# Kernel tuning notes

Hardware: AMD Instinct MI355X
Metric: run time of the kernel (lower is better)

The kernel has to match this reference:

```python
import jax, jax.numpy as jnp
import numpy as np

B, S, D, DEPTH = 2, 2048, 1024, 4
NUM_LEAVES = 2 ** DEPTH          # 16
NUM_DEC = NUM_LEAVES - 1         # 15


def setup_inputs() -> dict:
    key = jax.random.key(0)
    k1, k2, k3, k4, k5 = jax.random.split(key, 5)
    scale = 1.0 / np.sqrt(D)
    return {
        "x": jax.random.normal(k1, (B, S, D), dtype=jnp.float32),
        "dec_w": jax.random.normal(k2, (NUM_DEC, D), dtype=jnp.float32) * scale,
        "dec_b": jax.random.normal(k3, (NUM_DEC,), dtype=jnp.float32) * scale,
        "leaf_w": jax.random.normal(k4, (NUM_LEAVES, D, D), dtype=jnp.float32) * scale,  # [leaf, out, in] (torch Linear layout)
        "leaf_b": jax.random.normal(k5, (NUM_LEAVES, D), dtype=jnp.float32) * scale,
    }


def reference(x, dec_w, dec_b, leaf_w, leaf_b):
    num_leaves = leaf_w.shape[0]
    num_dec = num_leaves - 1
    # All decision-node sigmoids in one batched GEMM: [B,S,num_dec]
    dec = jax.nn.sigmoid(jnp.einsum("bsd,nd->bsn", x, dec_w) + dec_b)
    # Faithful to the original: each tree slot is multiplied exactly once by its
    # direct parent's decision (left child: p, right child: 1-p).
    leaf_idx = np.arange(num_dec, 2 * num_leaves - 1)      # slots holding leaf probs
    parent = (leaf_idx - 1) // 2                           # [num_leaves]
    is_left = (leaf_idx % 2 == 1)                          # [num_leaves]
    dec_p = dec[..., parent]                               # [B,S,num_leaves]
    leaf_probs = jnp.where(jnp.asarray(is_left), dec_p, 1.0 - dec_p)
    # All leaf MLPs as one batched GEMM: [B,S,L,D]
    leaf_out = jnp.einsum("bsd,lod->bslo", x, leaf_w) + leaf_b
    # Probability-weighted sum over leaves -> [B,S,D]
    return jnp.einsum("bslo,bsl->bso", leaf_out, leaf_probs)
```

## Files before the change

### kernel.cpp

```cpp
#include <hip/hip_runtime.h>
#include <stdint.h>


#define M_TOK 4096
#define DDIM  1024
#define KFLAT 9216

typedef __bf16 bf16x8 __attribute__((ext_vector_type(8)));
typedef float  f32x4  __attribute__((ext_vector_type(4)));
typedef unsigned short u16x4 __attribute__((ext_vector_type(4)));
typedef unsigned short u16x8 __attribute__((ext_vector_type(8)));

#define GLB(p) ((const __attribute__((address_space(1))) void*)(p))
#define LDS(p) ((__attribute__((address_space(3))) void*)(p))

__device__ __forceinline__ unsigned short f2bf(float f) {
    union { float f; uint32_t u; } v; v.f = f;
    uint32_t u = v.u;
    return (unsigned short)((u + 0x7fffu + ((u >> 16) & 1u)) >> 16);
}

__device__ __forceinline__ bf16x8 asbf(f32x4 v) {
    bf16x8 r; __builtin_memcpy(&r, &v, 16); return r;
}

template<int OFF>
__device__ __forceinline__ f32x4 dsr(uint32_t a) {
    f32x4 r;
    asm volatile("ds_read_b128 %0, %1 offset:%c2" : "=v"(r) : "v"(a), "i"(OFF));
    return r;
}

__global__ __launch_bounds__(256) void prep_dec_kernel(
    const float* __restrict__ x, const float* __restrict__ dec_w,
    const float* __restrict__ dec_b, const float* __restrict__ lw,
    const float* __restrict__ lb, unsigned short* __restrict__ wp,
    float* __restrict__ bw, unsigned short* __restrict__ xs,
    float* __restrict__ pmat, int newlay)
{
    if (blockIdx.x < 1024) {
        int idx = blockIdx.x * 256 + threadIdx.x;
        int o  = idx >> 8;
        int k4 = (idx & 255) << 2;
        size_t src = (size_t)o * DDIM + k4;
        const int nt = o >> 8, wn = (o >> 6) & 3, jj = (o >> 4) & 3, ra = o & 15;
        auto store4 = [&](int l, u16x4 d) {
            if (newlay) {
                int K    = l * DDIM + k4;
                int kt   = K >> 6;
                int half = (K >> 5) & 1;
                int g16  = (K >> 3) & 3;
                int e0   = K & 7;
                size_t a = ((size_t)(nt * 144 + kt) * 4 + wn) * 4096
                         + (jj * 2 + half) * 512 + (g16 * 16 + ra) * 8 + e0;
                *(u16x4*)(wp + a) = d;
            } else {
                *(u16x4*)(wp + (size_t)o * KFLAT + l * DDIM + k4) = d;
            }
        };
        float4 acc = make_float4(0.f, 0.f, 0.f, 0.f);
#pragma unroll
        for (int j = 0; j < 8; ++j) {
            const float4 a = *(const float4*)(lw + (size_t)(2*j)   * DDIM*DDIM + src);
            const float4 b = *(const float4*)(lw + (size_t)(2*j+1) * DDIM*DDIM + src);
            u16x4 d;
            d[0] = f2bf(a.x - b.x); d[1] = f2bf(a.y - b.y);
            d[2] = f2bf(a.z - b.z); d[3] = f2bf(a.w - b.w);
            store4(j, d);
            acc.x += b.x; acc.y += b.y; acc.z += b.z; acc.w += b.w;
        }
        u16x4 s;
        s[0] = f2bf(acc.x); s[1] = f2bf(acc.y); s[2] = f2bf(acc.z); s[3] = f2bf(acc.w);
        store4(8, s);
        if ((idx & 255) == 0) {
            float sb = 0.f;
#pragma unroll
            for (int j = 0; j < 8; ++j) {
                float ba = lb[(2*j) * DDIM + o];
                float bb = lb[(2*j+1) * DDIM + o];
                bw[j * DDIM + o] = ba - bb;
                sb += bb;
            }
            bw[8 * DDIM + o] = sb;
        }
    } else {
        int m    = (blockIdx.x - 1024) * 4 + (threadIdx.x >> 6);
        int lane = threadIdx.x & 63;
        const float* xr = x + (size_t)m * DDIM + lane * 16;
        float xv[16];
        *(float4*)&xv[0]  = *(const float4*)(xr + 0);
        *(float4*)&xv[4]  = *(const float4*)(xr + 4);
        *(float4*)&xv[8]  = *(const float4*)(xr + 8);
        *(float4*)&xv[12] = *(const float4*)(xr + 12);
        float s[8];
#pragma unroll
        for (int j = 0; j < 8; ++j) {
            const float* wr = dec_w + (size_t)(7 + j) * DDIM + lane * 16;
            float a = 0.f;
#pragma unroll
            for (int i = 0; i < 16; i += 4) {
                float4 wv = *(const float4*)(wr + i);
                a = fmaf(xv[i], wv.x, fmaf(xv[i+1], wv.y, fmaf(xv[i+2], wv.z, fmaf(xv[i+3], wv.w, a))));
            }
            s[j] = a;
        }
#pragma unroll
        for (int j = 0; j < 8; ++j)
#pragma unroll
            for (int off = 32; off > 0; off >>= 1)
                s[j] += __shfl_xor(s[j], off);
        float p[8];
#pragma unroll
        for (int j = 0; j < 8; ++j)
            p[j] = 1.0f / (1.0f + expf(-(s[j] + dec_b[7 + j])));
        if (lane == 0) {
#pragma unroll
            for (int j = 0; j < 8; ++j)
                pmat[(size_t)m * 8 + j] = p[j];
        }
#pragma unroll
        for (int j = 0; j < 9; ++j) {
            float pj = (j < 8) ? p[j] : 1.0f;
            unsigned short* dst = xs + (size_t)m * KFLAT + j * DDIM + lane * 16;
#pragma unroll
            for (int c = 0; c < 2; ++c) {
                u16x8 o;
#pragma unroll
                for (int e = 0; e < 8; ++e) o[e] = f2bf(pj * xv[c * 8 + e]);
                *(u16x8*)(dst + c * 8) = o;
            }
        }
    }
}

#define WAITV0 asm volatile("s_waitcnt vmcnt(0)" ::: "memory")
#define WAITV4 asm volatile("s_waitcnt vmcnt(4)" ::: "memory")
#define WAITV8 asm volatile("s_waitcnt vmcnt(8)" ::: "memory")
#define BARR   __builtin_amdgcn_s_barrier()
#define SBAR   __builtin_amdgcn_sched_barrier(0)
#define LGKM0  do { asm volatile("s_waitcnt lgkmcnt(0)" ::: "memory"); SBAR; } while(0)
#define LGKM4  do { asm volatile("s_waitcnt lgkmcnt(4)" ::: "memory"); SBAR; } while(0)

#define MFMA_Q(q, ASET, BSET) do { \
    __builtin_amdgcn_s_setprio(1); \
    _Pragma("unroll") \
    for (int mfl = 0; mfl < 2; ++mfl) { \
        _Pragma("unroll") \
        for (int j = 0; j < 4; ++j) { \
            acc[2*(q)+mfl][j] = __builtin_amdgcn_mfma_f32_16x16x32_bf16(asbf(ASET[mfl][0]), asbf(BSET[j][0]), acc[2*(q)+mfl][j], 0, 0, 0); \
            acc[2*(q)+mfl][j] = __builtin_amdgcn_mfma_f32_16x16x32_bf16(asbf(ASET[mfl][1]), asbf(BSET[j][1]), acc[2*(q)+mfl][j], 0, 0, 0); \
        } \
    } \
    __builtin_amdgcn_s_setprio(0); \
} while(0)

#define READ_A(SET, q, a0, a1) do { \
    SET[0][0] = dsr<(2*(q)+0)*2048>(a0); \
    SET[0][1] = dsr<(2*(q)+0)*2048>(a1); \
    SET[1][0] = dsr<(2*(q)+1)*2048>(a0); \
    SET[1][1] = dsr<(2*(q)+1)*2048>(a1); \
} while(0)

#define READ_B(SET, b0, b1) do { \
    SET[0][0] = dsr<0*2048>(b0); SET[0][1] = dsr<0*2048>(b1); \
    SET[1][0] = dsr<1*2048>(b0); SET[1][1] = dsr<1*2048>(b1); \
    SET[2][0] = dsr<2*2048>(b0); SET[2][1] = dsr<2*2048>(b1); \
    SET[3][0] = dsr<3*2048>(b0); SET[3][1] = dsr<3*2048>(b1); \
} while(0)

__global__ __launch_bounds__(512, 2) void tree_gemm9(
    const unsigned short* __restrict__ xs,
    const unsigned short* __restrict__ wpf,
    float* __restrict__ out, float* __restrict__ parts)
{
    extern __shared__ char smem[];
    const int tid  = threadIdx.x;
    const int lane = tid & 63;
    const int w    = tid >> 6;
    const int wm   = w >> 2, wn = w & 3;
    const int ra   = lane & 15;
    const int g16  = lane >> 4;

    const int flat = blockIdx.x;
    const int xcd  = flat & 7;
    const int idx  = flat >> 3;
    const int cc   = idx >> 4;
    const int mt   = idx & 15;
    const int code = xcd * 2 + cc;
    const int nt   = code >> 2;
    const int g    = code & 3;
    const int m0   = mt * 256, n0 = nt * 256;
    const int k0   = g * 2304;
    const int NT   = 36;

    uint32_t sbase = (uint32_t)(uintptr_t)(__attribute__((address_space(3))) char*)smem;
    const uint32_t colb0 = (uint32_t)((g16 ^ (ra & 7)) << 4);
    const uint32_t colb1 = colb0 ^ 64;
    const uint32_t baseA0s = sbase + wm * 16384 + ra * 128 + colb0;
    const uint32_t baseA1s = sbase + wm * 16384 + ra * 128 + colb1;

    const int kel = (((lane & 7) ^ (lane >> 3)) & 7) * 8;
    const int rA  = w * 8 + (lane >> 3);

    auto stageA = [&](int buf, int tt, int hh) {
        const unsigned short* s0 = xs + (size_t)(m0 + hh * 128 + rA) * KFLAT + (k0 + tt * 64 + kel);
        char* d0 = smem + buf * 32768 + hh * 16384 + w * 1024;
        __builtin_amdgcn_global_load_lds(GLB(s0), LDS(d0), 16, 0, 0);
        __builtin_amdgcn_global_load_lds(GLB(s0 + (size_t)64 * KFLAT), LDS(d0 + 8192), 16, 0, 0);
    };

    const unsigned short* bsrc = wpf
        + ((size_t)(nt * 144 + g * 36) * 4 + wn) * 4096 + lane * 8;

    f32x4 acc[8][4] = {};
    f32x4 avA[2][2], avB[2][2], bvX[4][2], bvY[4][2];

    auto loadB = [&](f32x4 (&SET)[4][2], const unsigned short* bp) {
#pragma unroll
        for (int j = 0; j < 4; ++j) {
            SET[j][0] = *(const f32x4*)(bp + (j * 2 + 0) * 512);
            SET[j][1] = *(const f32x4*)(bp + (j * 2 + 1) * 512);
        }
    };

    stageA(0, 0, 0); stageA(0, 0, 1);
    loadB(bvX, bsrc);
    WAITV0;
    BARR;
    READ_A(avA, 0, baseA0s, baseA1s);

#define TILE_BODY(T, CUR, NXT) do { \
    const int t_ = (T); \
    const bool s1 = (t_ + 1 < NT); \
    if (s1) { \
        stageA((t_ + 1) & 1, t_ + 1, 0); stageA((t_ + 1) & 1, t_ + 1, 1); \
        loadB(NXT, bsrc + 16384); \
    } \
    const uint32_t a0_ = baseA0s + ((uint32_t)(t_ & 1) << 15); \
    const uint32_t a1_ = baseA1s + ((uint32_t)(t_ & 1) << 15); \
    READ_A(avB, 1, a0_, a1_); \
    LGKM4;  MFMA_Q(0, avA, CUR); \
    READ_A(avA, 2, a0_, a1_); \
    LGKM4;  MFMA_Q(1, avB, CUR); \
    READ_A(avB, 3, a0_, a1_); \
    LGKM4;  MFMA_Q(2, avA, CUR); \
    LGKM0; \
    if (s1) { \
        WAITV0; \
        BARR; \
        const uint32_t na0_ = baseA0s + ((uint32_t)((t_ + 1) & 1) << 15); \
        const uint32_t na1_ = baseA1s + ((uint32_t)((t_ + 1) & 1) << 15); \
        READ_A(avA, 0, na0_, na1_); \
    } \
    MFMA_Q(3, avB, CUR); \
    SBAR; \
    bsrc += 16384; \
} while(0)

    for (int tp = 0; tp < NT; tp += 2) {
        TILE_BODY(tp,     bvX, bvY);
        TILE_BODY(tp + 1, bvY, bvX);
    }
#undef TILE_BODY

    float* dst = (g == 0) ? out : parts + (size_t)(g - 1) * M_TOK * DDIM;
#pragma unroll
    for (int mf = 0; mf < 8; ++mf)
#pragma unroll
        for (int e = 0; e < 4; ++e) {
            int row = m0 + wm * 128 + mf * 16 + g16 * 4 + e;
#pragma unroll
            for (int j = 0; j < 4; ++j)
                dst[(size_t)row * DDIM + n0 + wn * 64 + j * 16 + ra] = acc[mf][j][e];
        }
}

__global__ __launch_bounds__(256) void reduce2_kernel(
    float* __restrict__ out, const float* __restrict__ parts,
    const float* __restrict__ pmat, const float* __restrict__ bw, int np)
{
    size_t i = (size_t)blockIdx.x * 256 + threadIdx.x;
    int m   = (int)(i >> 8);
    int col = (int)(i & 255) * 4;
    float4 a = ((const float4*)out)[i];
    for (int p = 0; p < np; ++p) {
        float4 b = ((const float4*)(parts + (size_t)p * M_TOK * DDIM))[i];
        a.x += b.x; a.y += b.y; a.z += b.z; a.w += b.w;
    }
    float4 pa = *(const float4*)(pmat + (size_t)m * 8);
    float4 pb = *(const float4*)(pmat + (size_t)m * 8 + 4);
    float4 bias = *(const float4*)(bw + 8 * DDIM + col);
#pragma unroll
    for (int l = 0; l < 8; ++l) {
        float pl = (l < 4) ? ((const float*)&pa)[l] : ((const float*)&pb)[l - 4];
        float4 bl = *(const float4*)(bw + l * DDIM + col);
        bias.x = fmaf(pl, bl.x, bias.x); bias.y = fmaf(pl, bl.y, bias.y);
        bias.z = fmaf(pl, bl.z, bias.z); bias.w = fmaf(pl, bl.w, bias.w);
    }
    a.x += bias.x; a.y += bias.y; a.z += bias.z; a.w += bias.w;
    ((float4*)out)[i] = a;
}

__global__ __launch_bounds__(512, 2) void tree_gemm8(
    const unsigned short* __restrict__ xs, const unsigned short* __restrict__ wp,
    float* __restrict__ out, float* __restrict__ parts, int KG)
{
    extern __shared__ char smem[];
    const int tid  = threadIdx.x;
    const int lane = tid & 63;
    const int w    = tid >> 6;
    const int wm   = w >> 2, wn = w & 3;
    const int ra   = lane & 15;
    const int g16  = lane >> 4;

    const int bx  = blockIdx.x;
    const int xcd = bx & 7, ii = bx >> 3;
    const int nt  = xcd >> 1;
    const int mt  = (xcd & 1) * 8 + ii;
    const int m0  = mt * 256, n0 = nt * 256;
    const int g   = blockIdx.y;
    const int k0  = g * KG;
    const int NT  = KG >> 6;

    uint32_t sbase = (uint32_t)(uintptr_t)(__attribute__((address_space(3))) char*)smem;
    const uint32_t colb0 = (uint32_t)((g16 ^ (ra & 7)) << 4);
    const uint32_t colb1 = colb0 ^ 64;
    const uint32_t baseA0s = sbase + wm * 16384 + ra * 128 + colb0;
    const uint32_t baseA1s = sbase + wm * 16384 + ra * 128 + colb1;
    const uint32_t baseB0s = sbase + 65536 + wn * 8192 + ra * 128 + colb0;
    const uint32_t baseB1s = sbase + 65536 + wn * 8192 + ra * 128 + colb1;

    const int kel = (((lane & 7) ^ (lane >> 3)) & 7) * 8;
    const int rA  = w * 8 + (lane >> 3);

    auto stageA = [&](int buf, int tt, int hh) {
        const unsigned short* s0 = xs + (size_t)(m0 + hh * 128 + rA) * KFLAT + (k0 + tt * 64 + kel);
        char* d0 = smem + buf * 32768 + hh * 16384 + w * 1024;
        __builtin_amdgcn_global_load_lds(GLB(s0), LDS(d0), 16, 0, 0);
        __builtin_amdgcn_global_load_lds(GLB(s0 + (size_t)64 * KFLAT), LDS(d0 + 8192), 16, 0, 0);
    };
    auto stageB = [&](int buf, int tt, int hh) {
        const unsigned short* s0 = wp + (size_t)(n0 + hh * 128 + rA) * KFLAT + (k0 + tt * 64 + kel);
        char* d0 = smem + 65536 + buf * 32768 + hh * 16384 + w * 1024;
        __builtin_amdgcn_global_load_lds(GLB(s0), LDS(d0), 16, 0, 0);
        __builtin_amdgcn_global_load_lds(GLB(s0 + (size_t)64 * KFLAT), LDS(d0 + 8192), 16, 0, 0);
    };

    f32x4 acc[8][4] = {};
    f32x4 avA[2][2], avB[2][2], bvX[4][2], bvY[4][2];

    stageA(0, 0, 0); stageA(0, 0, 1);
    stageB(0, 0, 0); stageB(0, 0, 1);
    stageB(1, 1, 0); stageB(1, 1, 1);
    WAITV4;
    BARR;
    READ_B(bvX, baseB0s, baseB1s);
    READ_A(avA, 0, baseA0s, baseA1s);

    int bt1 = 1, bt2 = 2;

#define TILE_BODY8(T, CUR, NXT) do { \
    const int t_ = (T); \
    const bool s1 = (t_ + 1 < NT), s2 = (t_ + 2 < NT); \
    if (s1) { stageA((t_ + 1) & 1, t_ + 1, 0); stageA((t_ + 1) & 1, t_ + 1, 1); } \
    if (s2) { stageB(bt2, t_ + 2, 0); stageB(bt2, t_ + 2, 1); } \
    const uint32_t a0_ = baseA0s + ((uint32_t)(t_ & 1) << 15); \
    const uint32_t a1_ = baseA1s + ((uint32_t)(t_ & 1) << 15); \
    READ_A(avB, 1, a0_, a1_); \
    LGKM4;  MFMA_Q(0, avA, CUR); \
    READ_A(avA, 2, a0_, a1_); \
    LGKM4;  MFMA_Q(1, avB, CUR); \
    READ_A(avB, 3, a0_, a1_); \
    LGKM4;  MFMA_Q(2, avA, CUR); \
    LGKM0; \
    if (s1) { \
        if (s2) { WAITV4; } else { WAITV0; } \
        BARR; \
        const uint32_t nb0_ = baseB0s + (uint32_t)bt1 * 32768u; \
        const uint32_t nb1_ = baseB1s + (uint32_t)bt1 * 32768u; \
        const uint32_t na0_ = baseA0s + ((uint32_t)((t_ + 1) & 1) << 15); \
        const uint32_t na1_ = baseA1s + ((uint32_t)((t_ + 1) & 1) << 15); \
        READ_B(NXT, nb0_, nb1_); \
        READ_A(avA, 0, na0_, na1_); \
    } \
    MFMA_Q(3, avB, CUR); \
    SBAR; \
    bt1 = (bt1 == 2) ? 0 : bt1 + 1; \
    bt2 = (bt2 == 2) ? 0 : bt2 + 1; \
} while(0)

    for (int tp = 0; tp < NT; tp += 2) {
        TILE_BODY8(tp,     bvX, bvY);
        TILE_BODY8(tp + 1, bvY, bvX);
    }
#undef TILE_BODY8

    float* dst = (g == 0) ? out : parts + (size_t)(g - 1) * M_TOK * DDIM;
#pragma unroll
    for (int mf = 0; mf < 8; ++mf)
#pragma unroll
        for (int e = 0; e < 4; ++e) {
            int row = m0 + wm * 128 + mf * 16 + g16 * 4 + e;
#pragma unroll
            for (int j = 0; j < 4; ++j)
                dst[(size_t)row * DDIM + n0 + wn * 64 + j * 16 + ra] = acc[mf][j][e];
        }
}

__global__ __launch_bounds__(256, 4) void tree_gemm3(
    const unsigned short* __restrict__ xs, const unsigned short* __restrict__ wp,
    const float* __restrict__ bw, const float* __restrict__ pmat,
    float* __restrict__ out, float* __restrict__ parts, int KG)
{
    __shared__ __align__(16) unsigned short Asm[2][128 * 32];
    __shared__ __align__(16) unsigned short Bsm[2][128 * 32];
    const int tid  = threadIdx.x;
    const int lane = tid & 63;
    const int w    = tid >> 6;
    const int wm   = w >> 1, wn = w & 1;
    const int bx   = blockIdx.x;
    const int xcd  = bx & 7;
    const int ii   = bx >> 3;
    const int mt   = xcd * 4 + (ii >> 3);
    const int nt   = ii & 7;
    const int m0   = mt * 128, n0 = nt * 128;
    const int g    = blockIdx.y;
    const int k0   = g * KG;
    const int ra   = lane & 15;
    const int kb   = (lane >> 4) * 8;
    f32x4 acc[4][4] = {};
    auto stage = [&](int buf, int t) {
#pragma unroll
        for (int c = 0; c < 2; ++c) {
            int row = w * 32 + c * 16 + (lane >> 2);
            int ke  = k0 + t * 32 + (lane & 3) * 8;
            const unsigned short* ga = xs + (size_t)(m0 + row) * KFLAT + ke;
            __builtin_amdgcn_global_load_lds(GLB(ga), LDS(&Asm[buf][w * 1024 + c * 512]), 16, 0, 0);
            const unsigned short* gb = wp + (size_t)(n0 + row) * KFLAT + ke;
            __builtin_amdgcn_global_load_lds(GLB(gb), LDS(&Bsm[buf][w * 1024 + c * 512]), 16, 0, 0);
        }
    };
    const int TOT = KG >> 5;
    stage(0, 0);
    __syncthreads();
    int cur = 0;
    for (int t = 0; t < TOT; ++t) {
        if (t + 1 < TOT) stage(cur ^ 1, t + 1);
        bf16x8 av2[4], bv2[4];
#pragma unroll
        for (int i2 = 0; i2 < 4; ++i2)
            av2[i2] = *(const bf16x8*)&Asm[cur][(wm * 64 + i2 * 16 + ra) * 32 + kb];
#pragma unroll
        for (int j = 0; j < 4; ++j)
            bv2[j] = *(const bf16x8*)&Bsm[cur][(wn * 64 + j * 16 + ra) * 32 + kb];
#pragma unroll
        for (int i2 = 0; i2 < 4; ++i2)
#pragma unroll
            for (int j = 0; j < 4; ++j)
                acc[i2][j] = __builtin_amdgcn_mfma_f32_16x16x32_bf16(av2[i2], bv2[j], acc[i2][j], 0, 0, 0);
        __syncthreads();
        cur ^= 1;
    }
    float* bsm = (float*)&Asm[0][0];
    if (g == 0) {
        for (int idx = tid; idx < 9 * 128; idx += 256)
            bsm[idx] = bw[(idx >> 7) * DDIM + n0 + (idx & 127)];
    }
    __syncthreads();
    float* dst = (g == 0) ? out : parts + (size_t)(g - 1) * M_TOK * DDIM;
#pragma unroll
    for (int i2 = 0; i2 < 4; ++i2)
#pragma unroll
        for (int r = 0; r < 4; ++r) {
            int row = m0 + wm * 64 + i2 * 16 + (lane >> 4) * 4 + r;
            float4 pa, pb;
            if (g == 0) {
                pa = *(const float4*)(pmat + (size_t)row * 8);
                pb = *(const float4*)(pmat + (size_t)row * 8 + 4);
            }
#pragma unroll
            for (int j = 0; j < 4; ++j) {
                int cl = wn * 64 + j * 16 + ra;
                float v = acc[i2][j][r];
                if (g == 0) {
                    v += pa.x * bsm[0 * 128 + cl] + pa.y * bsm[1 * 128 + cl]
                       + pa.z * bsm[2 * 128 + cl] + pa.w * bsm[3 * 128 + cl]
                       + pb.x * bsm[4 * 128 + cl] + pb.y * bsm[5 * 128 + cl]
                       + pb.z * bsm[6 * 128 + cl] + pb.w * bsm[7 * 128 + cl]
                       + bsm[8 * 128 + cl];
                }
                dst[(size_t)row * DDIM + n0 + cl] = v;
            }
        }
}

__global__ __launch_bounds__(256) void reduce_kernel(
    float* __restrict__ out, const float* __restrict__ parts, int np)
{
    size_t i = (size_t)blockIdx.x * 256 + threadIdx.x;
    float4 a = ((const float4*)out)[i];
    for (int p = 0; p < np; ++p) {
        float4 b = ((const float4*)(parts + (size_t)p * M_TOK * DDIM))[i];
        a.x += b.x; a.y += b.y; a.z += b.z; a.w += b.w;
    }
    ((float4*)out)[i] = a;
}

extern "C" void kernel_launch(void* const* d_in, const int* in_sizes, int n_in,
                              void* d_out, int out_size, void* d_ws, size_t ws_size,
                              hipStream_t stream) {
    (void)in_sizes; (void)n_in; (void)out_size;
    const float* x     = (const float*)d_in[0];
    const float* dec_w = (const float*)d_in[1];
    const float* dec_b = (const float*)d_in[2];
    const float* lw    = (const float*)d_in[3];
    const float* lb    = (const float*)d_in[4];
    float* out = (float*)d_out;
    uint8_t* w8 = (uint8_t*)d_ws;

    unsigned short* xs   = (unsigned short*)(w8);
    unsigned short* wp   = (unsigned short*)(w8 + 75497472);
    float*          bw   = (float*)(w8 + 94371840);
    float*          pmat = (float*)(w8 + 94408704);
    float*          parts= (float*)(w8 + 94539776);
    const size_t NEED3 = 94539776 + 2ull * 16777216;
    const size_t NEED4 = 94539776 + 3ull * 16777216;

    int ks = (ws_size >= NEED4) ? 4 : (ws_size >= NEED3) ? 3 : 0;
    if (!ks) return;

    bool use9 = false;
    if (ks == 4) {
        hipError_t e9 = hipFuncSetAttribute(
            reinterpret_cast<const void*>(tree_gemm9),
            hipFuncAttributeMaxDynamicSharedMemorySize, 65536);
        use9 = (e9 == hipSuccess);
    }

    prep_dec_kernel<<<2048, 256, 0, stream>>>(x, dec_w, dec_b, lw, lb, wp, bw, xs, pmat,
                                              use9 ? 1 : 0);

    if (use9) {
        tree_gemm9<<<256, 512, 65536, stream>>>(xs, wp, out, parts);
        reduce2_kernel<<<4096, 256, 0, stream>>>(out, parts, pmat, bw, 3);
        return;
    }

    hipError_t e8 = hipFuncSetAttribute(
        reinterpret_cast<const void*>(tree_gemm8),
        hipFuncAttributeMaxDynamicSharedMemorySize, 163840);
    if (e8 == hipSuccess) {
        tree_gemm8<<<dim3(64, ks), 512, 163840, stream>>>(xs, wp, out, parts, KFLAT / ks);
        reduce2_kernel<<<4096, 256, 0, stream>>>(out, parts, pmat, bw, ks - 1);
    } else {
        tree_gemm3<<<dim3(256, ks), 256, 0, stream>>>(xs, wp, bw, pmat, out, parts, KFLAT / ks);
        reduce_kernel<<<4096, 256, 0, stream>>>(out, parts, ks - 1);
    }
}
```

Before: 137.2 us.

## Switch main GEMM to 32x32x16 MFMA with matching B layout and relaxed waits

Replaces the 16x16x32 MFMA GEMM kernel with a 32x32x16 variant. The prep kernel writes the packed weight layout to match the new fragment shape, and the LDS A-read swizzle is reorganized into four k-slices. The vmcnt waits are relaxed (vmcnt(12)/vmcnt(8) instead of vmcnt(0)) so global prefetch overlaps more with compute. The goal is fewer LDS reads per FLOP and higher MFMA throughput, at the cost of larger accumulator register pressure and a scattered epilogue store pattern.

```diff
diff --git a/kernel.cpp b/kernel.cpp
--- a/kernel.cpp
+++ b/kernel.cpp
@@ -8,6 +8,7 @@
 
 typedef __bf16 bf16x8 __attribute__((ext_vector_type(8)));
 typedef float  f32x4  __attribute__((ext_vector_type(4)));
+typedef float  f32x16 __attribute__((ext_vector_type(16)));
 typedef unsigned short u16x4 __attribute__((ext_vector_type(4)));
 typedef unsigned short u16x8 __attribute__((ext_vector_type(8)));
 
@@ -43,16 +44,16 @@
         int o  = idx >> 8;
         int k4 = (idx & 255) << 2;
         size_t src = (size_t)o * DDIM + k4;
-        const int nt = o >> 8, wn = (o >> 6) & 3, jj = (o >> 4) & 3, ra = o & 15;
+        const int nt = o >> 8, wn = (o >> 6) & 3, nf = (o >> 5) & 1, c31 = o & 31;
         auto store4 = [&](int l, u16x4 d) {
             if (newlay) {
-                int K    = l * DDIM + k4;
-                int kt   = K >> 6;
-                int half = (K >> 5) & 1;
-                int g16  = (K >> 3) & 3;
-                int e0   = K & 7;
+                int K  = l * DDIM + k4;
+                int kt = K >> 6;
+                int ks = (K >> 4) & 3;
+                int h  = (K >> 3) & 1;
+                int e0 = K & 7;
                 size_t a = ((size_t)(nt * 144 + kt) * 4 + wn) * 4096
-                         + (jj * 2 + half) * 512 + (g16 * 16 + ra) * 8 + e0;
+                         + (nf * 4 + ks) * 512 + (h * 32 + c31) * 8 + e0;
                 *(u16x4*)(wp + a) = d;
             } else {
                 *(u16x4*)(wp + (size_t)o * KFLAT + l * DDIM + k4) = d;
@@ -140,6 +141,159 @@
 #define SBAR   __builtin_amdgcn_sched_barrier(0)
 #define LGKM0  do { asm volatile("s_waitcnt lgkmcnt(0)" ::: "memory"); SBAR; } while(0)
 #define LGKM4  do { asm volatile("s_waitcnt lgkmcnt(4)" ::: "memory"); SBAR; } while(0)
+#define WV12LG4 do { asm volatile("s_waitcnt vmcnt(12) lgkmcnt(4)" ::: "memory"); SBAR; } while(0)
+#define WV0LG4  do { asm volatile("s_waitcnt vmcnt(0) lgkmcnt(4)" ::: "memory"); SBAR; } while(0)
+
+#define RA10(SET, AD) do { \
+    SET[0] = dsr<0>(AD); SET[1] = dsr<4096>(AD); \
+    SET[2] = dsr<8192>(AD); SET[3] = dsr<12288>(AD); \
+} while(0)
+
+#define MFMA_KS(ks, BS, AS) do { \
+    __builtin_amdgcn_s_setprio(1); \
+    _Pragma("unroll") \
+    for (int mf = 0; mf < 4; ++mf) { \
+        _Pragma("unroll") \
+        for (int nf = 0; nf < 2; ++nf) \
+            acc[mf][nf] = __builtin_amdgcn_mfma_f32_32x32x16_bf16( \
+                asbf(AS[mf]), asbf(BS[nf][ks]), acc[mf][nf], 0, 0, 0); \
+    } \
+    __builtin_amdgcn_s_setprio(0); \
+} while(0)
+
+__global__ __launch_bounds__(512, 2) void tree_gemm10(
+    const unsigned short* __restrict__ xs,
+    const unsigned short* __restrict__ wpf,
+    float* __restrict__ out, float* __restrict__ parts)
+{
+    extern __shared__ char smem[];
+    const int tid  = threadIdx.x;
+    const int lane = tid & 63;
+    const int w    = tid >> 6;
+    const int wm   = w >> 2, wn = w & 3;
+    const int l31  = lane & 31;
+    const int lh   = lane >> 5;
+
+    const int flat = blockIdx.x;
+    const int xcd  = flat & 7;
+    const int idx  = flat >> 3;
+    const int cc   = idx >> 4;
+    const int mt   = idx & 15;
+    const int code = xcd * 2 + cc;
+    const int nt   = code >> 2;
+    const int g    = code & 3;
+    const int m0   = mt * 256, n0 = nt * 256;
+    const int k0   = g * 2304;
+    const int NT   = 36;
+
+    uint32_t sbase = (uint32_t)(uintptr_t)(__attribute__((address_space(3))) char*)smem;
+    uint32_t baseA[4];
+#pragma unroll
+    for (int ks = 0; ks < 4; ++ks)
+        baseA[ks] = sbase + wm * 16384 + (uint32_t)l31 * 128
+                  + (uint32_t)((((ks << 1) | lh) ^ (lane & 7)) << 4);
+
+    const int kel = (((lane & 7) ^ (lane >> 3)) & 7) * 8;
+    const int rA  = w * 8 + (lane >> 3);
+
+    auto stageA = [&](int buf, int tt, int hh) {
+        const unsigned short* s0 = xs + (size_t)(m0 + hh * 128 + rA) * KFLAT + (k0 + tt * 64 + kel);
+        char* d0 = smem + buf * 32768 + hh * 16384 + w * 1024;
+        __builtin_amdgcn_global_load_lds(GLB(s0), LDS(d0), 16, 0, 0);
+        __builtin_amdgcn_global_load_lds(GLB(s0 + (size_t)64 * KFLAT), LDS(d0 + 8192), 16, 0, 0);
+    };
+
+    const unsigned short* bsrc = wpf
+        + ((size_t)(nt * 144 + g * 36) * 4 + wn) * 4096 + lane * 8;
+
+    f32x16 acc[4][2] = {};
+    f32x4 avX[4], avY[4], bvX[2][4], bvY[2][4];
+
+    auto loadB = [&](f32x4 (&SET)[2][4], const unsigned short* bp) {
+#pragma unroll
+        for (int nf = 0; nf < 2; ++nf)
+#pragma unroll
+            for (int ks = 0; ks < 4; ++ks)
+                SET[nf][ks] = *(const f32x4*)(bp + (nf * 4 + ks) * 512);
+    };
+
+    stageA(0, 0, 0); stageA(0, 0, 1);
+    loadB(bvX, bsrc);
+    WAITV0;
+    BARR;
+    RA10(avX, baseA[0]);
+
+#define TILE_BODY10(T, CUR, NXT) do { \
+    const int t_ = (T); \
+    const bool s1 = (t_ + 1 < NT); \
+    if (s1) { \
+        stageA((t_ + 1) & 1, t_ + 1, 0); stageA((t_ + 1) & 1, t_ + 1, 1); \
+        loadB(NXT, bsrc + 16384); \
+    } \
+    const uint32_t aoff = (uint32_t)(t_ & 1) << 15; \
+    RA10(avY, baseA[1] + aoff); \
+    if (s1) { WV12LG4; } else { WV0LG4; } \
+    MFMA_KS(0, CUR, avX); \
+    RA10(avX, baseA[2] + aoff); \
+    LGKM4;  MFMA_KS(1, CUR, avY); \
+    RA10(avY, baseA[3] + aoff); \
+    LGKM4;  MFMA_KS(2, CUR, avX); \
+    LGKM0; \
+    if (s1) { \
+        WAITV8; \
+        BARR; \
+        RA10(avX, baseA[0] + (aoff ^ 32768u)); \
+    } \
+    MFMA_KS(3, CUR, avY); \
+    SBAR; \
+    bsrc += 16384; \
+} while(0)
+
+    for (int tp = 0; tp < NT; tp += 2) {
+        TILE_BODY10(tp,     bvX, bvY);
+        TILE_BODY10(tp + 1, bvY, bvX);
+    }
+#undef TILE_BODY10
+
+    float* dst = (g == 0) ? out : parts + (size_t)(g - 1) * M_TOK * DDIM;
+#pragma unroll
+    for (int mf = 0; mf < 4; ++mf)
+#pragma unroll
+        for (int nf = 0; nf < 2; ++nf) {
+            int col = n0 + wn * 64 + nf * 32 + l31;
+#pragma unroll
+            for (int reg = 0; reg < 16; ++reg) {
+                int row = m0 + wm * 128 + mf * 32 + 4 * lh + (reg & 3) + 8 * (reg >> 2);
+                dst[(size_t)row * DDIM + col] = acc[mf][nf][reg];
+            }
+        }
+}
+
+__global__ __launch_bounds__(256) void reduce2_kernel(
+    float* __restrict__ out, const float* __restrict__ parts,
+    const float* __restrict__ pmat, const float* __restrict__ bw, int np)
+{
+    size_t i = (size_t)blockIdx.x * 256 + threadIdx.x;
+    int m   = (int)(i >> 8);
+    int col = (int)(i & 255) * 4;
+    float4 a = ((const float4*)out)[i];
+    for (int p = 0; p < np; ++p) {
+        float4 b = ((const float4*)(parts + (size_t)p * M_TOK * DDIM))[i];
+        a.x += b.x; a.y += b.y; a.z += b.z; a.w += b.w;
+    }
+    float4 pa = *(const float4*)(pmat + (size_t)m * 8);
+    float4 pb = *(const float4*)(pmat + (size_t)m * 8 + 4);
+    float4 bias = *(const float4*)(bw + 8 * DDIM + col);
+#pragma unroll
+    for (int l = 0; l < 8; ++l) {
+        float pl = (l < 4) ? ((const float*)&pa)[l] : ((const float*)&pb)[l - 4];
+        float4 bl = *(const float4*)(bw + l * DDIM + col);
+        bias.x = fmaf(pl, bl.x, bias.x); bias.y = fmaf(pl, bl.y, bias.y);
+        bias.z = fmaf(pl, bl.z, bias.z); bias.w = fmaf(pl, bl.w, bias.w);
+    }
+    a.x += bias.x; a.y += bias.y; a.z += bias.z; a.w += bias.w;
+    ((float4*)out)[i] = a;
+}
 
 #define MFMA_Q(q, ASET, BSET) do { \
     __builtin_amdgcn_s_setprio(1); \
@@ -167,139 +321,6 @@
     SET[2][0] = dsr<2*2048>(b0); SET[2][1] = dsr<2*2048>(b1); \
     SET[3][0] = dsr<3*2048>(b0); SET[3][1] = dsr<3*2048>(b1); \
 } while(0)
-
-__global__ __launch_bounds__(512, 2) void tree_gemm9(
-    const unsigned short* __restrict__ xs,
-    const unsigned short* __restrict__ wpf,
-    float* __restrict__ out, float* __restrict__ parts)
-{
-    extern __shared__ char smem[];
-    const int tid  = threadIdx.x;
-    const int lane = tid & 63;
-    const int w    = tid >> 6;
-    const int wm   = w >> 2, wn = w & 3;
-    const int ra   = lane & 15;
-    const int g16  = lane >> 4;
-
-    const int flat = blockIdx.x;
-    const int xcd  = flat & 7;
-    const int idx  = flat >> 3;
-    const int cc   = idx >> 4;
-    const int mt   = idx & 15;
-    const int code = xcd * 2 + cc;
-    const int nt   = code >> 2;
-    const int g    = code & 3;
-    const int m0   = mt * 256, n0 = nt * 256;
-    const int k0   = g * 2304;
-    const int NT   = 36;
-
-    uint32_t sbase = (uint32_t)(uintptr_t)(__attribute__((address_space(3))) char*)smem;
-    const uint32_t colb0 = (uint32_t)((g16 ^ (ra & 7)) << 4);
-    const uint32_t colb1 = colb0 ^ 64;
-    const uint32_t baseA0s = sbase + wm * 16384 + ra * 128 + colb0;
-    const uint32_t baseA1s = sbase + wm * 16384 + ra * 128 + colb1;
-
-    const int kel = (((lane & 7) ^ (lane >> 3)) & 7) * 8;
-    const int rA  = w * 8 + (lane >> 3);
-
-    auto stageA = [&](int buf, int tt, int hh) {
-        const unsigned short* s0 = xs + (size_t)(m0 + hh * 128 + rA) * KFLAT + (k0 + tt * 64 + kel);
-        char* d0 = smem + buf * 32768 + hh * 16384 + w * 1024;
-        __builtin_amdgcn_global_load_lds(GLB(s0), LDS(d0), 16, 0, 0);
-        __builtin_amdgcn_global_load_lds(GLB(s0 + (size_t)64 * KFLAT), LDS(d0 + 8192), 16, 0, 0);
-    };
-
-    const unsigned short* bsrc = wpf
-        + ((size_t)(nt * 144 + g * 36) * 4 + wn) * 4096 + lane * 8;
-
-    f32x4 acc[8][4] = {};
-    f32x4 avA[2][2], avB[2][2], bvX[4][2], bvY[4][2];
-
-    auto loadB = [&](f32x4 (&SET)[4][2], const unsigned short* bp) {
-#pragma unroll
-        for (int j = 0; j < 4; ++j) {
-            SET[j][0] = *(const f32x4*)(bp + (j * 2 + 0) * 512);
-            SET[j][1] = *(const f32x4*)(bp + (j * 2 + 1) * 512);
-        }
-    };
-
-    stageA(0, 0, 0); stageA(0, 0, 1);
-    loadB(bvX, bsrc);
-    WAITV0;
-    BARR;
-    READ_A(avA, 0, baseA0s, baseA1s);
-
-#define TILE_BODY(T, CUR, NXT) do { \
-    const int t_ = (T); \
-    const bool s1 = (t_ + 1 < NT); \
-    if (s1) { \
-        stageA((t_ + 1) & 1, t_ + 1, 0); stageA((t_ + 1) & 1, t_ + 1, 1); \
-        loadB(NXT, bsrc + 16384); \
-    } \
-    const uint32_t a0_ = baseA0s + ((uint32_t)(t_ & 1) << 15); \
-    const uint32_t a1_ = baseA1s + ((uint32_t)(t_ & 1) << 15); \
-    READ_A(avB, 1, a0_, a1_); \
-    LGKM4;  MFMA_Q(0, avA, CUR); \
-    READ_A(avA, 2, a0_, a1_); \
-    LGKM4;  MFMA_Q(1, avB, CUR); \
-    READ_A(avB, 3, a0_, a1_); \
-    LGKM4;  MFMA_Q(2, avA, CUR); \
-    LGKM0; \
-    if (s1) { \
-        WAITV0; \
-        BARR; \
-        const uint32_t na0_ = baseA0s + ((uint32_t)((t_ + 1) & 1) << 15); \
-        const uint32_t na1_ = baseA1s + ((uint32_t)((t_ + 1) & 1) << 15); \
-        READ_A(avA, 0, na0_, na1_); \
-    } \
-    MFMA_Q(3, avB, CUR); \
-    SBAR; \
-    bsrc += 16384; \
-} while(0)
-
-    for (int tp = 0; tp < NT; tp += 2) {
-        TILE_BODY(tp,     bvX, bvY);
-        TILE_BODY(tp + 1, bvY, bvX);
-    }
-#undef TILE_BODY
-
-    float* dst = (g == 0) ? out : parts + (size_t)(g - 1) * M_TOK * DDIM;
-#pragma unroll
-    for (int mf = 0; mf < 8; ++mf)
-#pragma unroll
-        for (int e = 0; e < 4; ++e) {
-            int row = m0 + wm * 128 + mf * 16 + g16 * 4 + e;
-#pragma unroll
-            for (int j = 0; j < 4; ++j)
-                dst[(size_t)row * DDIM + n0 + wn * 64 + j * 16 + ra] = acc[mf][j][e];
-        }
-}
-
-__global__ __launch_bounds__(256) void reduce2_kernel(
-    float* __restrict__ out, const float* __restrict__ parts,
-    const float* __restrict__ pmat, const float* __restrict__ bw, int np)
-{
-    size_t i = (size_t)blockIdx.x * 256 + threadIdx.x;
-    int m   = (int)(i >> 8);
-    int col = (int)(i & 255) * 4;
-    float4 a = ((const float4*)out)[i];
-    for (int p = 0; p < np; ++p) {
-        float4 b = ((const float4*)(parts + (size_t)p * M_TOK * DDIM))[i];
-        a.x += b.x; a.y += b.y; a.z += b.z; a.w += b.w;
-    }
-    float4 pa = *(const float4*)(pmat + (size_t)m * 8);
-    float4 pb = *(const float4*)(pmat + (size_t)m * 8 + 4);
-    float4 bias = *(const float4*)(bw + 8 * DDIM + col);
-#pragma unroll
-    for (int l = 0; l < 8; ++l) {
-        float pl = (l < 4) ? ((const float*)&pa)[l] : ((const float*)&pb)[l - 4];
-        float4 bl = *(const float4*)(bw + l * DDIM + col);
-        bias.x = fmaf(pl, bl.x, bias.x); bias.y = fmaf(pl, bl.y, bias.y);
-        bias.z = fmaf(pl, bl.z, bias.z); bias.w = fmaf(pl, bl.w, bias.w);
-    }
-    a.x += bias.x; a.y += bias.y; a.z += bias.z; a.w += bias.w;
-    ((float4*)out)[i] = a;
-}
 
 __global__ __launch_bounds__(512, 2) void tree_gemm8(
     const unsigned short* __restrict__ xs, const unsigned short* __restrict__ wp,
@@ -529,19 +550,19 @@
     int ks = (ws_size >= NEED4) ? 4 : (ws_size >= NEED3) ? 3 : 0;
     if (!ks) return;
 
-    bool use9 = false;
+    bool use10 = false;
     if (ks == 4) {
-        hipError_t e9 = hipFuncSetAttribute(
-            reinterpret_cast<const void*>(tree_gemm9),
+        hipError_t e10 = hipFuncSetAttribute(
+            reinterpret_cast<const void*>(tree_gemm10),
             hipFuncAttributeMaxDynamicSharedMemorySize, 65536);
-        use9 = (e9 == hipSuccess);
+        use10 = (e10 == hipSuccess);
     }
 
     prep_dec_kernel<<<2048, 256, 0, stream>>>(x, dec_w, dec_b, lw, lb, wp, bw, xs, pmat,
-                                              use9 ? 1 : 0);
-
-    if (use9) {
-        tree_gemm9<<<256, 512, 65536, stream>>>(xs, wp, out, parts);
+                                              use10 ? 1 : 0);
+
+    if (use10) {
+        tree_gemm10<<<256, 512, 65536, stream>>>(xs, wp, out, parts);
         reduce2_kernel<<<4096, 256, 0, stream>>>(out, parts, pmat, bw, 3);
         return;
     }
```

Result: slower. 143.8 us (+4.8%).
